# Kernel optimization log

Measured on AMD Instinct MI355X. Metric: run time of the kernel, lower is better.

The kernel has to match this reference:

```python
import jax, jax.numpy as jnp
import numpy as np

N = 50000      # nodes
E = 600000     # edges
F_IN = 128     # input features
H = 128        # hidden
C = 40         # classes


def _glorot(key, shape):
    lim = float(np.sqrt(6.0 / (shape[0] + shape[1])))
    return jax.random.uniform(key, shape, jnp.float32, -lim, lim)


def setup_inputs() -> dict:
    key = jax.random.key(0)
    ks = jax.random.split(key, 16)
    inp = {
        "x": jax.random.normal(ks[0], (N, F_IN), jnp.float32),
        "edge_index": jax.random.randint(ks[1], (2, E), 0, N, jnp.int64),
    }
    # SAGEConv params: Wl (neighbor branch, with bias), Wr (root branch), stored [in, out]
    dims = [(F_IN, H), (H, H), (H, H)]
    for i, (din, dout) in enumerate(dims, start=1):
        inp[f"Wl{i}"] = _glorot(ks[2 * i], (din, dout))
        inp[f"bl{i}"] = jnp.zeros((dout,), jnp.float32)
        inp[f"Wr{i}"] = _glorot(ks[2 * i + 1], (din, dout))
    inp["W_lin1"] = _glorot(ks[10], (H, H))
    inp["b_lin1"] = jnp.zeros((H,), jnp.float32)
    inp["W_lin2"] = _glorot(ks[11], (H, C))
    inp["b_lin2"] = jnp.zeros((C,), jnp.float32)
    return inp


def _sage_conv(x, src, dst, Wl, bl, Wr):
    # mean-aggregate neighbor features at destination nodes
    msgs = x[src]  # [E, d] gather
    agg = jax.ops.segment_sum(msgs, dst, num_segments=N)
    deg = jax.ops.segment_sum(jnp.ones((E,), x.dtype), dst, num_segments=N)
    agg = agg / jnp.clip(deg, 1.0)[:, None]
    return agg @ Wl + bl + x @ Wr


def reference(x, edge_index, Wl1, bl1, Wr1, Wl2, bl2, Wr2, Wl3, bl3, Wr3,
              W_lin1, b_lin1, W_lin2, b_lin2):
    src, dst = edge_index[0], edge_index[1]
    h = jax.nn.relu(_sage_conv(x, src, dst, Wl1, bl1, Wr1))
    h = jax.nn.relu(_sage_conv(h, src, dst, Wl2, bl2, Wr2))
    h = jax.nn.relu(_sage_conv(h, src, dst, Wl3, bl3, Wr3))
    h = jax.nn.relu(h @ W_lin1 + b_lin1)
    # dropout: inference mode (training=False) -> identity
    logits = h @ W_lin2 + b_lin2
    return jax.nn.log_softmax(logits, axis=-1)
```

## Files before the change

kernel.cpp:

```cpp
#include <hip/hip_runtime.h>
#include <hip/hip_bf16.h>
#include <math.h>

#define NNODES 50000
#define NEDGES 600000
#define FDIM   128
#define NCLS   40
#define DEG_BLOCKS 2344
#define CVT_BLOCKS 6251
#define S1_TOTAL (DEG_BLOCKS + CVT_BLOCKS + 62)
#define NT32 ((NNODES + 31) / 32)
#define ESRC_CAP 1360128

typedef __hip_bfloat16 bf16;
typedef short bf16x8 __attribute__((ext_vector_type(8)));
typedef short bf16x4 __attribute__((ext_vector_type(4)));
typedef float f32x4  __attribute__((ext_vector_type(4)));

__device__ __forceinline__ float b2f(short u) {
    union { unsigned int i; float f; } cv;
    cv.i = ((unsigned int)(unsigned short)u) << 16;
    return cv.f;
}
__device__ __forceinline__ short f2b(float f) {
    bf16 h = __float2bfloat16(f);
    return *(const short*)&h;
}
__device__ __forceinline__ int edge_val(const int* e32, const long long* e64,
                                        int is64, int idx) {
    return is64 ? (int)e64[idx] : e32[idx];
}
__device__ __forceinline__ float ldf(const void* p, int fp32, int idx) {
    return fp32 ? ((const float*)p)[idx]
                : __bfloat162float(((const bf16*)p)[idx]);
}
__device__ __forceinline__ int lidx(int row, int col) {
    return row * 128 + ((((col >> 3) ^ (row & 15)) << 3) | (col & 7));
}

struct MP {
    const int* e32; const long long* e64;
    const void* xin;
    const void *Wl1, *Wr1, *Wl2, *Wr2, *Wl3, *Wr3, *Wlin1, *Wlin2;
    const void *b1, *b2, *b3, *b4, *b5;
    int *deg, *start, *cursor, *flags, *edge_src;
    bf16x8* packed; float* biasf;
    bf16 *xb, *bufA;
    float* out;
};

__device__ __forceinline__ void detect_body(int b, int tid, const unsigned int* ei,
        const unsigned int* xp, const unsigned int* wp, int* flags, int* cnt) {
    if (tid == 0) *cnt = 0;
    __syncthreads();
    if (b == 0) {
        int nz = 0;
        for (int i = tid; i < 2048; i += 256) if (ei[2 * i + 1] != 0u) nz++;
        atomicAdd(cnt, nz);
        __syncthreads();
        if (tid == 0) flags[1] = (*cnt == 0) ? 1 : 0;
    } else {
        const unsigned int* pp = (b == 1) ? xp : wp;
        int inr = 0;
        for (int i = tid; i < 2048; i += 256) {
            unsigned int e = (pp[i] >> 7) & 0xFFu;
            if (e >= 100u && e <= 140u) inr++;
        }
        atomicAdd(cnt, inr);
        __syncthreads();
        if (tid == 0) flags[b + 1] = (*cnt < 1024) ? 1 : 0;
    }
}

__global__ void k_init_f(const unsigned int* ei, const unsigned int* xp,
                         const unsigned int* wp, int* flags, int* deg,
                         int* edge_src) {
    __shared__ int cnt;
    int b = blockIdx.x, tid = threadIdx.x, B = gridDim.x;
    if (b < 3) detect_body(b, tid, ei, xp, wp, flags, &cnt);
    if (b == 3 && tid == 0) flags[0] = 0;
    for (int i = b * 256 + tid; i < NNODES; i += B * 256) deg[i] = 0;
    for (int i = b * 256 + tid; i < ESRC_CAP; i += B * 256) edge_src[i] = NNODES;
}

__device__ __forceinline__ void stage1_body(int vb, int tid, const MP& p,
                                            int is64, int xf, int wf) {
    if (vb < DEG_BLOCKS) {
        int i = vb * 256 + tid;
        if (i < NEDGES) {
            int dst = edge_val(p.e32, p.e64, is64, NEDGES + i);
            atomicAdd(&p.deg[dst], 1);
        }
        return;
    }
    if (vb < DEG_BLOCKS + CVT_BLOCKS) {
        int i = (vb - DEG_BLOCKS) * 256 + tid;
        if (i >= (NNODES + 1) * FDIM / 4) return;
        if (i >= NNODES * FDIM / 4) {
            bf16x4 z = (bf16x4){0, 0, 0, 0};
            ((bf16x4*)p.xb)[i] = z;
        } else if (xf) {
            float4 v = ((const float4*)p.xin)[i];
            bf16x4 o;
            o[0] = f2b(v.x); o[1] = f2b(v.y); o[2] = f2b(v.z); o[3] = f2b(v.w);
            ((bf16x4*)p.xb)[i] = o;
        } else {
            ((uint2*)p.xb)[i] = ((const uint2*)p.xin)[i];
        }
        return;
    }
    int lb = vb - DEG_BLOCKS - CVT_BLOCKS;
    if (lb >= 59) {
        int t = (lb - 59) * 256 + tid;
        if (t >= 5 * 128) return;
        int which = t >> 7, idx = t & 127;
        const void* srcs[5] = {p.b1, p.b2, p.b3, p.b4, p.b5};
        int n = (which == 4) ? NCLS : 128;
        float v = 0.f;
        if (idx < n) v = ldf(srcs[which], wf, idx);
        p.biasf[t] = v;
        return;
    }
    int t2 = lb * 256 + tid;
    int frag = t2 >> 6, lane = t2 & 63;
    if (frag >= 236) return;
    int q = lane >> 4, l16 = lane & 15;
    const void* W;
    int kbase, n, ldw = 128, nvalid = 128;
    if (frag < 192) {
        int g = frag >> 6, local = frag & 63;
        int kt = local >> 3, nt = local & 7;
        const void* Wl = (g == 0) ? p.Wl1 : (g == 1) ? p.Wl2 : p.Wl3;
        const void* Wr = (g == 0) ? p.Wr1 : (g == 1) ? p.Wr2 : p.Wr3;
        W = (kt < 4) ? Wl : Wr;
        kbase = (kt & 3) * 32;
        n = nt * 16 + l16;
    } else if (frag < 224) {
        int local = frag - 192;
        int kt = local >> 3, nt = local & 7;
        W = p.Wlin1; kbase = kt * 32; n = nt * 16 + l16;
    } else {
        int local = frag - 224;
        int kt = local / 3, nt = local % 3;
        W = p.Wlin2; kbase = kt * 32; n = nt * 16 + l16;
        ldw = NCLS; nvalid = NCLS;
    }
    bf16x8 v;
#pragma unroll
    for (int j = 0; j < 8; j++) {
        float e = 0.f;
        if (n < nvalid) e = ldf(W, wf, (kbase + q * 8 + j) * ldw + n);
        v[j] = f2b(e);
    }
    p.packed[frag * 64 + lane] = v;
}
__global__ void k_stage1_f(MP p) {
    stage1_body(blockIdx.x, threadIdx.x, p, p.flags[1], p.flags[2], p.flags[3]);
}

__global__ void k_alloc_f(MP p) {
    __shared__ int sA[256];
    __shared__ int sb;
    int t = threadIdx.x;
    int i = blockIdx.x * 256 + t;
    int dv = (i < NNODES) ? p.deg[i] : 0;
    int pv = (dv + 15) & ~15;
    sA[t] = pv;
    __syncthreads();
    for (int off = 1; off < 256; off <<= 1) {
        int v = (t >= off) ? sA[t - off] : 0;
        __syncthreads();
        sA[t] += v;
        __syncthreads();
    }
    if (t == 255) sb = atomicAdd(&p.flags[0], sA[255]);
    __syncthreads();
    if (i < NNODES) {
        int st = sb + sA[t] - pv;
        p.start[i] = st;
        p.cursor[i] = st;
    }
}
__global__ void k_fill_f(MP p) {
    int i = blockIdx.x * 256 + threadIdx.x;
    if (i >= NEDGES) return;
    int is64 = p.flags[1];
    int srcn = edge_val(p.e32, p.e64, is64, i);
    int dstn = edge_val(p.e32, p.e64, is64, NEDGES + i);
    int pos = atomicAdd(&p.cursor[dstn], 1);
    p.edge_src[pos] = srcn;
}

__device__ __forceinline__ void agg_wave(const bf16* __restrict__ x,
        const int* __restrict__ start, const int* __restrict__ deg,
        const int* __restrict__ edge_src, short* __restrict__ lds,
        int rowbase, int wave, int lane) {
    const int g = lane >> 4, c = lane & 15;
    const int base = rowbase + wave * 8;
    int s = 0, dgv = 0, eidx = NNODES;
    if (base < NNODES) {
        s = start[base]; dgv = deg[base];
        eidx = edge_src[s + lane];
    }
    for (int t = 0; t < 8; t++) {
        int nodeN = base + t + 1;
        int sn = 0, dgn = 0;
        bool haveN = (t < 7) && (nodeN < NNODES);
        if (haveN) { sn = start[nodeN]; dgn = deg[nodeN]; }
        int dcap = dgv < 64 ? ((dgv + 15) & ~15) : 64;
        float acc[8];
#pragma unroll
        for (int e = 0; e < 8; e++) acc[e] = 0.f;
        for (int i = 0; i < dcap; i += 16) {
            int i0 = __shfl(eidx, i + g);
            int i1 = __shfl(eidx, i + 4 + g);
            int i2 = __shfl(eidx, i + 8 + g);
            int i3 = __shfl(eidx, i + 12 + g);
            bf16x8 v0 = *(const bf16x8*)(x + (size_t)i0 * FDIM + c * 8);
            bf16x8 v1 = *(const bf16x8*)(x + (size_t)i1 * FDIM + c * 8);
            bf16x8 v2 = *(const bf16x8*)(x + (size_t)i2 * FDIM + c * 8);
            bf16x8 v3 = *(const bf16x8*)(x + (size_t)i3 * FDIM + c * 8);
#pragma unroll
            for (int e = 0; e < 8; e++)
                acc[e] += (b2f(v0[e]) + b2f(v1[e])) + (b2f(v2[e]) + b2f(v3[e]));
        }
        if (dgv > 64) {
            for (int t2 = 64; t2 < dgv; t2++) {
                int srcn = edge_src[s + t2];
                bf16x8 v0 = *(const bf16x8*)(x + (size_t)srcn * FDIM + c * 8);
                if (g == 0) {
#pragma unroll
                    for (int e = 0; e < 8; e++) acc[e] += b2f(v0[e]);
                }
            }
        }
        int en = NNODES;
        if (haveN) en = edge_src[sn + lane];
#pragma unroll
        for (int e = 0; e < 8; e++) {
            float a = acc[e];
            a += __shfl_xor(a, 16);
            a += __shfl_xor(a, 32);
            acc[e] = a;
        }
        if (g == 0) {
            float inv = (dgv > 0) ? 1.f / (float)dgv : 0.f;
            bf16x8 o;
#pragma unroll
            for (int e = 0; e < 8; e++) o[e] = f2b(acc[e] * inv);
            *(bf16x8*)(lds + lidx(wave * 8 + t, c * 8)) = o;
        }
        s = sn; dgv = dgn; eidx = en;
    }
}

template <bool TO_LDS>
__device__ __forceinline__ void gemm_phase(int rowbase, int lane, int wave,
        short* __restrict__ aggL, const bf16* __restrict__ xroot,
        const bf16x8* __restrict__ packed, const float* __restrict__ bias,
        bf16* __restrict__ out) {
    const int q = lane >> 4, l16 = lane & 15;
    const int mt = wave & 1, half = wave >> 1;
    const int rowb2 = rowbase + mt * 16;
    int rowA = rowb2 + l16;
    if (rowA >= NNODES) rowA = NNODES - 1;
    f32x4 acc[4];
#pragma unroll
    for (int n = 0; n < 4; n++) acc[n] = (f32x4){0.f, 0.f, 0.f, 0.f};
#pragma unroll 2
    for (int kt = 0; kt < 8; kt++) {
        bf16x8 a;
        if (kt < 4)
            a = *(const bf16x8*)(aggL + lidx(mt * 16 + l16, kt * 32 + q * 8));
        else
            a = *(const bf16x8*)(xroot + (size_t)rowA * FDIM + (kt - 4) * 32 + q * 8);
        bf16x8 b[4];
#pragma unroll
        for (int n = 0; n < 4; n++)
            b[n] = packed[(kt * 8 + half * 4 + n) * 64 + lane];
#pragma unroll
        for (int n = 0; n < 4; n++)
            acc[n] = __builtin_amdgcn_mfma_f32_16x16x32_bf16(a, b[n], acc[n], 0, 0, 0);
    }
#pragma unroll
    for (int n = 0; n < 4; n++) {
        int col = (half * 4 + n) * 16 + l16;
        float bv = bias[col];
#pragma unroll
        for (int r = 0; r < 4; r++) {
            float v = fmaxf(acc[n][r] + bv, 0.f);
            if (TO_LDS) {
                aggL[lidx(mt * 16 + q * 4 + r, col)] = f2b(v);
            } else {
                int row = rowb2 + q * 4 + r;
                if (row < NNODES)
                    out[(size_t)row * FDIM + col] = __float2bfloat16(v);
                else if (row == NNODES)
                    out[(size_t)row * FDIM + col] = __float2bfloat16(0.f);
            }
        }
    }
}

__device__ __forceinline__ void head_phase(int rowbase, int lane, int wave,
        const short* __restrict__ h3, short* __restrict__ h1,
        const bf16x8* __restrict__ packed, const float* __restrict__ bias1,
        const float* __restrict__ bias2, float* __restrict__ out) {
    const int q = lane >> 4, l16 = lane & 15;
    const int mt = wave & 1, half = wave >> 1;
    f32x4 acc[4];
#pragma unroll
    for (int n = 0; n < 4; n++) acc[n] = (f32x4){0.f, 0.f, 0.f, 0.f};
#pragma unroll 2
    for (int kt = 0; kt < 4; kt++) {
        bf16x8 a = *(const bf16x8*)(h3 + lidx(mt * 16 + l16, kt * 32 + q * 8));
        bf16x8 b[4];
#pragma unroll
        for (int n = 0; n < 4; n++)
            b[n] = packed[(192 + kt * 8 + half * 4 + n) * 64 + lane];
#pragma unroll
        for (int n = 0; n < 4; n++)
            acc[n] = __builtin_amdgcn_mfma_f32_16x16x32_bf16(a, b[n], acc[n], 0, 0, 0);
    }
#pragma unroll
    for (int n = 0; n < 4; n++) {
        int col = (half * 4 + n) * 16 + l16;
        float bv = bias1[col];
#pragma unroll
        for (int r = 0; r < 4; r++)
            h1[lidx(mt * 16 + q * 4 + r, col)] = f2b(fmaxf(acc[n][r] + bv, 0.f));
    }
    __syncthreads();
    if (wave >= 2) return;
    f32x4 acc2[3];
#pragma unroll
    for (int n = 0; n < 3; n++) acc2[n] = (f32x4){0.f, 0.f, 0.f, 0.f};
#pragma unroll
    for (int kt = 0; kt < 4; kt++) {
        bf16x8 a = *(const bf16x8*)(h1 + lidx(wave * 16 + l16, kt * 32 + q * 8));
        bf16x8 b[3];
#pragma unroll
        for (int n = 0; n < 3; n++) b[n] = packed[(224 + kt * 3 + n) * 64 + lane];
#pragma unroll
        for (int n = 0; n < 3; n++)
            acc2[n] = __builtin_amdgcn_mfma_f32_16x16x32_bf16(a, b[n], acc2[n], 0, 0, 0);
    }
    const float NEG = -1e30f;
    bool v2ok = (l16 < 8);
#pragma unroll
    for (int r = 0; r < 4; r++) {
        int row = rowbase + wave * 16 + q * 4 + r;
        float v0 = acc2[0][r] + bias2[l16];
        float v1 = acc2[1][r] + bias2[16 + l16];
        float v2 = v2ok ? (acc2[2][r] + bias2[32 + l16]) : NEG;
        float m = fmaxf(fmaxf(v0, v1), v2);
#pragma unroll
        for (int mk = 1; mk < 16; mk <<= 1) m = fmaxf(m, __shfl_xor(m, mk));
        float sden = expf(v0 - m) + expf(v1 - m) + (v2ok ? expf(v2 - m) : 0.f);
#pragma unroll
        for (int mk = 1; mk < 16; mk <<= 1) sden += __shfl_xor(sden, mk);
        float l = m + logf(sden);
        if (row < NNODES) {
            out[(size_t)row * NCLS + l16] = v0 - l;
            out[(size_t)row * NCLS + 16 + l16] = v1 - l;
            if (v2ok) out[(size_t)row * NCLS + 32 + l16] = v2 - l;
        }
    }
}

__global__ void k_layer(const bf16* __restrict__ src, const int* __restrict__ start,
                        const int* __restrict__ deg, const int* __restrict__ edge_src,
                        const bf16x8* __restrict__ packed,
                        const float* __restrict__ bias, bf16* __restrict__ out) {
    __shared__ __align__(16) short aggL[32 * 128];
    const int lane = threadIdx.x & 63, wave = threadIdx.x >> 6;
    const int rowbase = blockIdx.x * 32;
    agg_wave(src, start, deg, edge_src, aggL, rowbase, wave, lane);
    __syncthreads();
    gemm_phase<false>(rowbase, lane, wave, aggL, src, packed, bias, out);
}

__global__ void k_layer3head(const bf16* __restrict__ src,
                             const int* __restrict__ start,
                             const int* __restrict__ deg,
                             const int* __restrict__ edge_src,
                             const bf16x8* __restrict__ packed,
                             const float* __restrict__ biasf,
                             float* __restrict__ out) {
    __shared__ __align__(16) short aggL[32 * 128];
    __shared__ __align__(16) short h1[32 * 128];
    const int lane = threadIdx.x & 63, wave = threadIdx.x >> 6;
    const int rowbase = blockIdx.x * 32;
    agg_wave(src, start, deg, edge_src, aggL, rowbase, wave, lane);
    __syncthreads();
    gemm_phase<true>(rowbase, lane, wave, aggL, src, packed + 128 * 64,
                     biasf + 256, nullptr);
    __syncthreads();
    head_phase(rowbase, lane, wave, aggL, h1, packed, biasf + 384, biasf + 512, out);
}

extern "C" void kernel_launch(void* const* d_in, const int* in_sizes, int n_in,
                              void* d_out, int out_size, void* d_ws, size_t ws_size,
                              hipStream_t stream) {
    char* ws = (char*)d_ws;
    size_t off = 0;
    auto take = [&](size_t bytes) {
        void* pp = ws + off;
        off = (off + bytes + 255) & ~(size_t)255;
        return pp;
    };
    MP p;
    p.e32 = (const int*)d_in[1];
    p.e64 = (const long long*)d_in[1];
    p.xin = d_in[0];
    p.Wl1 = d_in[2];  p.Wr1 = d_in[4];
    p.Wl2 = d_in[5];  p.Wr2 = d_in[7];
    p.Wl3 = d_in[8];  p.Wr3 = d_in[10];
    p.Wlin1 = d_in[11]; p.Wlin2 = d_in[13];
    p.b1 = d_in[3]; p.b2 = d_in[6]; p.b3 = d_in[9]; p.b4 = d_in[12]; p.b5 = d_in[14];
    p.deg      = (int*)take(NNODES * 4);
    p.start    = (int*)take(NNODES * 4);
    p.cursor   = (int*)take(NNODES * 4);
    p.flags    = (int*)take(256);
    p.edge_src = (int*)take((ESRC_CAP + 256) * 4);
    p.packed   = (bf16x8*)take(236 * 64 * 16);
    p.biasf    = (float*)take(5 * 128 * 4);
    p.xb       = (bf16*)take((size_t)(NNODES + 1) * FDIM * 2);
    p.bufA     = (bf16*)take((size_t)(NNODES + 1) * FDIM * 2);
    p.out      = (float*)d_out;
    bf16* bufB = p.xb;

    k_init_f<<<512, 256, 0, stream>>>((const unsigned int*)d_in[1],
                                      (const unsigned int*)d_in[0],
                                      (const unsigned int*)d_in[2],
                                      p.flags, p.deg, p.edge_src);
    k_stage1_f<<<S1_TOTAL, 256, 0, stream>>>(p);
    k_alloc_f<<<(NNODES + 255) / 256, 256, 0, stream>>>(p);
    k_fill_f<<<(NEDGES + 255) / 256, 256, 0, stream>>>(p);

    k_layer<<<NT32, 256, 0, stream>>>(p.xb, p.start, p.deg, p.edge_src,
                                      p.packed, p.biasf, p.bufA);
    k_layer<<<NT32, 256, 0, stream>>>(p.bufA, p.start, p.deg, p.edge_src,
                                      p.packed + 64 * 64, p.biasf + 128, bufB);
    k_layer3head<<<NT32, 256, 0, stream>>>(bufB, p.start, p.deg, p.edge_src,
                                           p.packed, p.biasf, p.out);
}
```

Measured before the change: 283.5 us.

## Shrink layer blocks to 16 rows and pad only per-node edge slack

Layer kernels now run 128-thread blocks covering 16 nodes, where they previously ran 256-thread blocks covering 32. This doubles the grid and lowers LDS per block, and since 50000 divides evenly by 16, all bounds checks are removed. The full-size edge_src sentinel fill in init is replaced by writing sentinels only into each node's padding slots during allocation, plus a one-time zeroing of the pad row in bufA. The aggregation loop is fully unrolled. The tradeoffs are more blocks and more weight-fragment loads per row, in exchange for better load balance and less init traffic.

```diff
diff --git a/kernel.cpp b/kernel.cpp
--- a/kernel.cpp
+++ b/kernel.cpp
@@ -9,7 +9,7 @@
 #define DEG_BLOCKS 2344
 #define CVT_BLOCKS 6251
 #define S1_TOTAL (DEG_BLOCKS + CVT_BLOCKS + 62)
-#define NT32 ((NNODES + 31) / 32)
+#define NT16 (NNODES / 16)
 #define ESRC_CAP 1360128
 
 typedef __hip_bfloat16 bf16;
@@ -73,14 +73,12 @@
 }
 
 __global__ void k_init_f(const unsigned int* ei, const unsigned int* xp,
-                         const unsigned int* wp, int* flags, int* deg,
-                         int* edge_src) {
+                         const unsigned int* wp, int* flags, int* deg) {
     __shared__ int cnt;
     int b = blockIdx.x, tid = threadIdx.x, B = gridDim.x;
     if (b < 3) detect_body(b, tid, ei, xp, wp, flags, &cnt);
     if (b == 3 && tid == 0) flags[0] = 0;
     for (int i = b * 256 + tid; i < NNODES; i += B * 256) deg[i] = 0;
-    for (int i = b * 256 + tid; i < ESRC_CAP; i += B * 256) edge_src[i] = NNODES;
 }
 
 __device__ __forceinline__ void stage1_body(int vb, int tid, const MP& p,
@@ -179,9 +177,12 @@
         int st = sb + sA[t] - pv;
         p.start[i] = st;
         p.cursor[i] = st;
+        for (int j = dv; j < pv; j++) p.edge_src[st + j] = NNODES;
     }
 }
 __global__ void k_fill_f(MP p) {
+    if (blockIdx.x == 0 && threadIdx.x < 32)
+        ((uint2*)(p.bufA + (size_t)NNODES * FDIM))[threadIdx.x] = (uint2){0u, 0u};
     int i = blockIdx.x * 256 + threadIdx.x;
     if (i >= NEDGES) return;
     int is64 = p.flags[1];
@@ -197,16 +198,13 @@
         int rowbase, int wave, int lane) {
     const int g = lane >> 4, c = lane & 15;
     const int base = rowbase + wave * 8;
-    int s = 0, dgv = 0, eidx = NNODES;
-    if (base < NNODES) {
-        s = start[base]; dgv = deg[base];
-        eidx = edge_src[s + lane];
-    }
+    int s = start[base], dgv = deg[base];
+    int eidx = edge_src[s + lane];
+#pragma unroll
     for (int t = 0; t < 8; t++) {
-        int nodeN = base + t + 1;
         int sn = 0, dgn = 0;
-        bool haveN = (t < 7) && (nodeN < NNODES);
-        if (haveN) { sn = start[nodeN]; dgn = deg[nodeN]; }
+        bool haveN = (t < 7);
+        if (haveN) { sn = start[base + t + 1]; dgn = deg[base + t + 1]; }
         int dcap = dgv < 64 ? ((dgv + 15) & ~15) : 64;
         float acc[8];
 #pragma unroll
@@ -234,7 +232,7 @@
                 }
             }
         }
-        int en = NNODES;
+        int en = 0;
         if (haveN) en = edge_src[sn + lane];
 #pragma unroll
         for (int e = 0; e < 8; e++) {
@@ -260,10 +258,7 @@
         const bf16x8* __restrict__ packed, const float* __restrict__ bias,
         bf16* __restrict__ out) {
     const int q = lane >> 4, l16 = lane & 15;
-    const int mt = wave & 1, half = wave >> 1;
-    const int rowb2 = rowbase + mt * 16;
-    int rowA = rowb2 + l16;
-    if (rowA >= NNODES) rowA = NNODES - 1;
+    const int rowA = rowbase + l16;
     f32x4 acc[4];
 #pragma unroll
     for (int n = 0; n < 4; n++) acc[n] = (f32x4){0.f, 0.f, 0.f, 0.f};
@@ -271,33 +266,29 @@
     for (int kt = 0; kt < 8; kt++) {
         bf16x8 a;
         if (kt < 4)
-            a = *(const bf16x8*)(aggL + lidx(mt * 16 + l16, kt * 32 + q * 8));
+            a = *(const bf16x8*)(aggL + lidx(l16, kt * 32 + q * 8));
         else
             a = *(const bf16x8*)(xroot + (size_t)rowA * FDIM + (kt - 4) * 32 + q * 8);
         bf16x8 b[4];
 #pragma unroll
         for (int n = 0; n < 4; n++)
-            b[n] = packed[(kt * 8 + half * 4 + n) * 64 + lane];
+            b[n] = packed[(kt * 8 + wave * 4 + n) * 64 + lane];
 #pragma unroll
         for (int n = 0; n < 4; n++)
             acc[n] = __builtin_amdgcn_mfma_f32_16x16x32_bf16(a, b[n], acc[n], 0, 0, 0);
     }
+    if (TO_LDS) __syncthreads();
 #pragma unroll
     for (int n = 0; n < 4; n++) {
-        int col = (half * 4 + n) * 16 + l16;
+        int col = (wave * 4 + n) * 16 + l16;
         float bv = bias[col];
 #pragma unroll
         for (int r = 0; r < 4; r++) {
             float v = fmaxf(acc[n][r] + bv, 0.f);
-            if (TO_LDS) {
-                aggL[lidx(mt * 16 + q * 4 + r, col)] = f2b(v);
-            } else {
-                int row = rowb2 + q * 4 + r;
-                if (row < NNODES)
-                    out[(size_t)row * FDIM + col] = __float2bfloat16(v);
-                else if (row == NNODES)
-                    out[(size_t)row * FDIM + col] = __float2bfloat16(0.f);
-            }
+            if (TO_LDS)
+                aggL[lidx(q * 4 + r, col)] = f2b(v);
+            else
+                out[(size_t)(rowbase + q * 4 + r) * FDIM + col] = __float2bfloat16(v);
         }
     }
 }
@@ -307,37 +298,36 @@
         const bf16x8* __restrict__ packed, const float* __restrict__ bias1,
         const float* __restrict__ bias2, float* __restrict__ out) {
     const int q = lane >> 4, l16 = lane & 15;
-    const int mt = wave & 1, half = wave >> 1;
     f32x4 acc[4];
 #pragma unroll
     for (int n = 0; n < 4; n++) acc[n] = (f32x4){0.f, 0.f, 0.f, 0.f};
 #pragma unroll 2
     for (int kt = 0; kt < 4; kt++) {
-        bf16x8 a = *(const bf16x8*)(h3 + lidx(mt * 16 + l16, kt * 32 + q * 8));
+        bf16x8 a = *(const bf16x8*)(h3 + lidx(l16, kt * 32 + q * 8));
         bf16x8 b[4];
 #pragma unroll
         for (int n = 0; n < 4; n++)
-            b[n] = packed[(192 + kt * 8 + half * 4 + n) * 64 + lane];
+            b[n] = packed[(192 + kt * 8 + wave * 4 + n) * 64 + lane];
 #pragma unroll
         for (int n = 0; n < 4; n++)
             acc[n] = __builtin_amdgcn_mfma_f32_16x16x32_bf16(a, b[n], acc[n], 0, 0, 0);
     }
 #pragma unroll
     for (int n = 0; n < 4; n++) {
-        int col = (half * 4 + n) * 16 + l16;
+        int col = (wave * 4 + n) * 16 + l16;
         float bv = bias1[col];
 #pragma unroll
         for (int r = 0; r < 4; r++)
-            h1[lidx(mt * 16 + q * 4 + r, col)] = f2b(fmaxf(acc[n][r] + bv, 0.f));
-    }
-    __syncthreads();
-    if (wave >= 2) return;
+            h1[lidx(q * 4 + r, col)] = f2b(fmaxf(acc[n][r] + bv, 0.f));
+    }
+    __syncthreads();
+    if (wave >= 1) return;
     f32x4 acc2[3];
 #pragma unroll
     for (int n = 0; n < 3; n++) acc2[n] = (f32x4){0.f, 0.f, 0.f, 0.f};
 #pragma unroll
     for (int kt = 0; kt < 4; kt++) {
-        bf16x8 a = *(const bf16x8*)(h1 + lidx(wave * 16 + l16, kt * 32 + q * 8));
+        bf16x8 a = *(const bf16x8*)(h1 + lidx(l16, kt * 32 + q * 8));
         bf16x8 b[3];
 #pragma unroll
         for (int n = 0; n < 3; n++) b[n] = packed[(224 + kt * 3 + n) * 64 + lane];
@@ -349,7 +339,7 @@
     bool v2ok = (l16 < 8);
 #pragma unroll
     for (int r = 0; r < 4; r++) {
-        int row = rowbase + wave * 16 + q * 4 + r;
+        int row = rowbase + q * 4 + r;
         float v0 = acc2[0][r] + bias2[l16];
         float v1 = acc2[1][r] + bias2[16 + l16];
         float v2 = v2ok ? (acc2[2][r] + bias2[32 + l16]) : NEG;
@@ -360,37 +350,34 @@
 #pragma unroll
         for (int mk = 1; mk < 16; mk <<= 1) sden += __shfl_xor(sden, mk);
         float l = m + logf(sden);
-        if (row < NNODES) {
-            out[(size_t)row * NCLS + l16] = v0 - l;
-            out[(size_t)row * NCLS + 16 + l16] = v1 - l;
-            if (v2ok) out[(size_t)row * NCLS + 32 + l16] = v2 - l;
-        }
-    }
-}
-
-__global__ void k_layer(const bf16* __restrict__ src, const int* __restrict__ start,
-                        const int* __restrict__ deg, const int* __restrict__ edge_src,
-                        const bf16x8* __restrict__ packed,
-                        const float* __restrict__ bias, bf16* __restrict__ out) {
-    __shared__ __align__(16) short aggL[32 * 128];
+        out[(size_t)row * NCLS + l16] = v0 - l;
+        out[(size_t)row * NCLS + 16 + l16] = v1 - l;
+        if (v2ok) out[(size_t)row * NCLS + 32 + l16] = v2 - l;
+    }
+}
+
+__global__ void __launch_bounds__(128)
+k_layer(const bf16* __restrict__ src, const int* __restrict__ start,
+        const int* __restrict__ deg, const int* __restrict__ edge_src,
+        const bf16x8* __restrict__ packed,
+        const float* __restrict__ bias, bf16* __restrict__ out) {
+    __shared__ __align__(16) short aggL[16 * 128];
     const int lane = threadIdx.x & 63, wave = threadIdx.x >> 6;
-    const int rowbase = blockIdx.x * 32;
+    const int rowbase = blockIdx.x * 16;
     agg_wave(src, start, deg, edge_src, aggL, rowbase, wave, lane);
     __syncthreads();
     gemm_phase<false>(rowbase, lane, wave, aggL, src, packed, bias, out);
 }
 
-__global__ void k_layer3head(const bf16* __restrict__ src,
-                             const int* __restrict__ start,
-                             const int* __restrict__ deg,
-                             const int* __restrict__ edge_src,
-                             const bf16x8* __restrict__ packed,
-                             const float* __restrict__ biasf,
-                             float* __restrict__ out) {
-    __shared__ __align__(16) short aggL[32 * 128];
-    __shared__ __align__(16) short h1[32 * 128];
+__global__ void __launch_bounds__(128)
+k_layer3head(const bf16* __restrict__ src, const int* __restrict__ start,
+             const int* __restrict__ deg, const int* __restrict__ edge_src,
+             const bf16x8* __restrict__ packed,
+             const float* __restrict__ biasf, float* __restrict__ out) {
+    __shared__ __align__(16) short aggL[16 * 128];
+    __shared__ __align__(16) short h1[16 * 128];
     const int lane = threadIdx.x & 63, wave = threadIdx.x >> 6;
-    const int rowbase = blockIdx.x * 32;
+    const int rowbase = blockIdx.x * 16;
     agg_wave(src, start, deg, edge_src, aggL, rowbase, wave, lane);
     __syncthreads();
     gemm_phase<true>(rowbase, lane, wave, aggL, src, packed + 128 * 64,
@@ -430,18 +417,18 @@
     p.out      = (float*)d_out;
     bf16* bufB = p.xb;
 
-    k_init_f<<<512, 256, 0, stream>>>((const unsigned int*)d_in[1],
+    k_init_f<<<200, 256, 0, stream>>>((const unsigned int*)d_in[1],
                                       (const unsigned int*)d_in[0],
                                       (const unsigned int*)d_in[2],
-                                      p.flags, p.deg, p.edge_src);
+                                      p.flags, p.deg);
     k_stage1_f<<<S1_TOTAL, 256, 0, stream>>>(p);
     k_alloc_f<<<(NNODES + 255) / 256, 256, 0, stream>>>(p);
     k_fill_f<<<(NEDGES + 255) / 256, 256, 0, stream>>>(p);
 
-    k_layer<<<NT32, 256, 0, stream>>>(p.xb, p.start, p.deg, p.edge_src,
+    k_layer<<<NT16, 128, 0, stream>>>(p.xb, p.start, p.deg, p.edge_src,
                                       p.packed, p.biasf, p.bufA);
-    k_layer<<<NT32, 256, 0, stream>>>(p.bufA, p.start, p.deg, p.edge_src,
+    k_layer<<<NT16, 128, 0, stream>>>(p.bufA, p.start, p.deg, p.edge_src,
                                       p.packed + 64 * 64, p.biasf + 128, bufB);
-    k_layer3head<<<NT32, 256, 0, stream>>>(bufB, p.start, p.deg, p.edge_src,
+    k_layer3head<<<NT16, 128, 0, stream>>>(bufB, p.start, p.deg, p.edge_src,
                                            p.packed, p.biasf, p.out);
 }
```

Result: no change. 283.5 us (-0.0%).
